# Optimization experiments

Hardware: AMD Instinct MI355X
Metric: run time of the kernel (lower is better)

## Reference

```python
import jax, jax.numpy as jnp
import numpy as np

HEADS = 12
DIM_HEAD = 64
SCALE = DIM_HEAD ** -0.5


def rotate_every_two(x):
    # (..., 2d) -> rotate pairs: (x1, x2) -> (-x2, x1)
    x = x.reshape(*x.shape[:-1], -1, 2)
    x1, x2 = x[..., 0], x[..., 1]
    return jnp.stack((-x2, x1), axis=-1).reshape(*x.shape[:-2], -1)


def apply_rotary_pos_emb(q, k, sinu_pos):
    # sinu_pos: (b, p, 2c) -> sin, cos each (b, p, c)
    b, p, two_c = sinu_pos.shape
    sp = sinu_pos.reshape(b, p, 2, two_c // 2)
    sin, cos = sp[:, :, 0, :], sp[:, :, 1, :]
    # interleave-repeat to (b, 1, p, 2c) to broadcast over heads
    sin = jnp.repeat(sin, 2, axis=-1)[:, None, :, :]
    cos = jnp.repeat(cos, 2, axis=-1)[:, None, :, :]
    rot = lambda t: t * cos + rotate_every_two(t) * sin
    return rot(q), rot(k)


def setup_inputs() -> dict:
    key = jax.random.key(0)
    ks = jax.random.split(key, 5)
    b, n, dim = 8, 1024, 768
    inner = HEADS * DIM_HEAD
    x = jax.random.normal(ks[0], (b, n, dim), dtype=jnp.float32)
    pos_emb = jax.random.normal(ks[1], (1, n, DIM_HEAD), dtype=jnp.float32)
    W_qkv = jax.random.normal(ks[2], (dim, 3 * inner), dtype=jnp.float32) * (dim ** -0.5)
    W_out = jax.random.normal(ks[3], (inner, dim), dtype=jnp.float32) * (inner ** -0.5)
    b_out = jnp.zeros((dim,), dtype=jnp.float32)
    return {"x": x, "pos_emb": pos_emb, "W_qkv": W_qkv, "W_out": W_out, "b_out": b_out}


def reference(x, pos_emb, W_qkv, W_out, b_out):
    b, n, _ = x.shape
    qkv = x @ W_qkv                                   # (b, n, 3*inner)
    q, k, v = jnp.split(qkv, 3, axis=-1)
    split_heads = lambda t: t.reshape(b, n, HEADS, DIM_HEAD).transpose(0, 2, 1, 3)
    q, k, v = split_heads(q), split_heads(k), split_heads(v)   # (b, h, n, d)
    q, k = apply_rotary_pos_emb(q, k, pos_emb)
    dots = jnp.einsum('bhid,bhjd->bhij', q, k) * SCALE
    attn = jax.nn.softmax(dots, axis=-1)
    out = jnp.einsum('bhij,bhjd->bhid', attn, v)
    out = out.transpose(0, 2, 1, 3).reshape(b, n, HEADS * DIM_HEAD)
    out = out @ W_out + b_out
    return out  # context is None -> torch code returns (out[:, :n], None); n == full length
```

## Files before the change

### kernel.cpp

```cpp
#include <hip/hip_runtime.h>
#include <hip/hip_bf16.h>

typedef __attribute__((ext_vector_type(8))) short bf16x8;
typedef __attribute__((ext_vector_type(4))) float f32x4;
typedef __attribute__((ext_vector_type(4))) unsigned short u16x4;
typedef unsigned short u16;
typedef unsigned int u32;

#define DEVINL __device__ __forceinline__

DEVINL u16 f2bf(float f) {
    union { float f; u32 u; } v; v.f = f;
    u32 r = v.u + 0x7FFFu + ((v.u >> 16) & 1u);
    return (u16)(r >> 16);
}
DEVINL float bf2f(u16 h) {
    union { u32 u; float f; } v; v.u = ((u32)h) << 16;
    return v.f;
}
DEVINL u32 cvt_pk_bf16(float lo, float hi) {
    u32 r;
    asm("v_cvt_pk_bf16_f32 %0, %1, %2" : "=v"(r) : "v"(lo), "v"(hi));
    return r;
}

#define GLOAD_LDS16(g, l) __builtin_amdgcn_global_load_lds( \
    (const __attribute__((address_space(1))) void*)(g), \
    (__attribute__((address_space(3))) void*)(l), 16, 0, 0)

#define SBAR() do { \
    __builtin_amdgcn_sched_barrier(0); \
    __builtin_amdgcn_s_barrier(); \
    __builtin_amdgcn_sched_barrier(0); } while (0)

__global__ void cvt_bf16_kernel(const float* __restrict__ in, u16* __restrict__ out, int n4) {
    int t = blockIdx.x * blockDim.x + threadIdx.x;
    if (t >= n4) return;
    const float4 v = reinterpret_cast<const float4*>(in)[t];
    u16x4 o;
    o[0] = f2bf(v.x); o[1] = f2bf(v.y); o[2] = f2bf(v.z); o[3] = f2bf(v.w);
    *reinterpret_cast<u16x4*>(out + (size_t)t * 4) = o;
}

__global__ __launch_bounds__(256) void transpose_cvt_kernel(const float* __restrict__ in,
                                                            u16* __restrict__ out,
                                                            int R, int C) {
    __shared__ float tile[32][33];
    int c0 = blockIdx.x * 32, r0 = blockIdx.y * 32;
    int tx = threadIdx.x & 31, ty = threadIdx.x >> 5;
#pragma unroll
    for (int i = 0; i < 4; ++i)
        tile[ty + i * 8][tx] = in[(size_t)(r0 + ty + i * 8) * C + c0 + tx];
    __syncthreads();
#pragma unroll
    for (int i = 0; i < 4; ++i)
        out[(size_t)(c0 + ty + i * 8) * R + r0 + tx] = f2bf(tile[tx][ty + i * 8]);
}

template<int NTN, int NFRAG, int BROWS, int K, bool BF16_OUT>
__global__ __launch_bounds__(512, 2) void gemm_bigtile_kernel(const u16* __restrict__ A,
                                                              const u16* __restrict__ Bt,
                                                              void* __restrict__ Cout,
                                                              const float* __restrict__ bias) {
    constexpr int BN = NFRAG * 32;
    constexpr int N = NTN * BN;
    constexpr int NT = K / 64;
    constexpr int APL = 256 * 64;
    constexpr int BPL = BROWS * 64;
    constexpr int BUFSZ = APL + BPL;
    constexpr int BCH = BROWS / 64;
    constexpr int TOT = 4 + BCH;
    __shared__ u16 lds[2 * BUFSZ];

    const int tid = threadIdx.x;
    const int wv = tid >> 6, lane = tid & 63;
    const int lr = lane & 15, lg = lane >> 4;
    const int wr = wv >> 1, wc = wv & 1;

    const int id = blockIdx.x;
    const int sid = (id & 7) * 32 + (id >> 3);
    const int bm = (sid / NTN) * 256;
    const int bn = (sid % NTN) * BN;

#define STAGE(nb_, kt_) do { \
    _Pragma("unroll") \
    for (int j_ = 0; j_ < 4; ++j_) { \
        const int idx_ = j_ * 512 + tid; \
        const int row_ = idx_ >> 3; \
        const int c_ = (idx_ & 7) ^ (row_ & 7); \
        GLOAD_LDS16(A + (size_t)(bm + row_) * K + (kt_) * 64 + c_ * 8, \
                    (char*)lds + ((nb_) * BUFSZ + (j_ * 512 + wv * 64) * 8) * 2); \
    } \
    _Pragma("unroll") \
    for (int j_ = 0; j_ < BCH; ++j_) { \
        const int idx_ = j_ * 512 + tid; \
        const int row_ = idx_ >> 3; \
        const int c_ = (idx_ & 7) ^ (row_ & 7); \
        GLOAD_LDS16(Bt + (size_t)(bn + row_) * K + (kt_) * 64 + c_ * 8, \
                    (char*)lds + ((nb_) * BUFSZ + APL + (j_ * 512 + wv * 64) * 8) * 2); \
    } } while (0)

#define COMPUTE(cur_) do { \
    _Pragma("unroll") \
    for (int ks_ = 0; ks_ < 2; ++ks_) { \
        bf16x8 af[4], bfr[NFRAG]; \
        _Pragma("unroll") \
        for (int mf_ = 0; mf_ < 4; ++mf_) { \
            const int row_ = wr * 64 + mf_ * 16 + lr; \
            af[mf_] = *reinterpret_cast<const bf16x8*>( \
                &lds[(cur_) * BUFSZ + row_ * 64 + (((ks_ * 4 + lg) ^ (row_ & 7)) * 8)]); \
        } \
        _Pragma("unroll") \
        for (int nf_ = 0; nf_ < NFRAG; ++nf_) { \
            const int row_ = wc * (NFRAG * 16) + nf_ * 16 + lr; \
            bfr[nf_] = *reinterpret_cast<const bf16x8*>( \
                &lds[(cur_) * BUFSZ + APL + row_ * 64 + (((ks_ * 4 + lg) ^ (row_ & 7)) * 8)]); \
        } \
        __builtin_amdgcn_s_setprio(1); \
        _Pragma("unroll") \
        for (int mf_ = 0; mf_ < 4; ++mf_) \
        _Pragma("unroll") \
        for (int nf_ = 0; nf_ < NFRAG; ++nf_) \
            acc[mf_][nf_] = __builtin_amdgcn_mfma_f32_16x16x32_bf16( \
                af[mf_], bfr[nf_], acc[mf_][nf_], 0, 0, 0); \
        __builtin_amdgcn_s_setprio(0); \
    } } while (0)

    f32x4 acc[4][NFRAG];
#pragma unroll
    for (int i = 0; i < 4; ++i)
#pragma unroll
        for (int j = 0; j < NFRAG; ++j) acc[i][j] = (f32x4){0.f, 0.f, 0.f, 0.f};

    STAGE(0, 0);
    for (int kt = 0; kt < NT - 1; ++kt) {
        const int cur = kt & 1;
        STAGE(cur ^ 1, kt + 1);
        __builtin_amdgcn_sched_barrier(0);
        if constexpr (TOT == 9) asm volatile("s_waitcnt vmcnt(9)" ::: "memory");
        else asm volatile("s_waitcnt vmcnt(6)" ::: "memory");
        SBAR();
        COMPUTE(cur);
        SBAR();
    }
    {
        const int cur = (NT - 1) & 1;
        __builtin_amdgcn_sched_barrier(0);
        asm volatile("s_waitcnt vmcnt(0)" ::: "memory");
        SBAR();
        COMPUTE(cur);
    }

#pragma unroll
    for (int mf = 0; mf < 4; ++mf)
#pragma unroll
        for (int nf = 0; nf < NFRAG; ++nf) {
            const int col = bn + wc * (NFRAG * 16) + nf * 16 + lr;
            const float bv = BF16_OUT ? 0.f : bias[col];
#pragma unroll
            for (int r = 0; r < 4; ++r) {
                const int row = bm + wr * 64 + mf * 16 + lg * 4 + r;
                if (BF16_OUT)
                    ((u16*)Cout)[(size_t)row * N + col] = f2bf(acc[mf][nf][r]);
                else
                    ((float*)Cout)[(size_t)row * N + col] = acc[mf][nf][r] + bv;
            }
        }
#undef STAGE
#undef COMPUTE
}

__global__ __launch_bounds__(256) void rot_vtrans_kernel(u16* __restrict__ qkv,
                                                         const float* __restrict__ pos,
                                                         u16* __restrict__ Vt) {
    __shared__ u16 tile[64][72];
    const int bid = blockIdx.x;
    if (bid < 6144) {
        int t = bid * 256 + threadIdx.x;
        int row = t / 192;
        int col = (t % 192) * 8;
        int n = row & 1023;
        int i0 = (col & 63) >> 1;
        const float qs = (col < 768) ? 0.18033688f : 1.0f;
        const float* pn = pos + (size_t)n * 64;
        u16* p = qkv + (size_t)row * 2304 + col;
        bf16x8 v = *reinterpret_cast<bf16x8*>(p);
        u16 o[8];
#pragma unroll
        for (int j = 0; j < 4; ++j) {
            float s = pn[i0 + j], c = pn[32 + i0 + j];
            float x0 = bf2f((u16)v[2 * j]), x1 = bf2f((u16)v[2 * j + 1]);
            o[2 * j]     = f2bf((x0 * c - x1 * s) * qs);
            o[2 * j + 1] = f2bf((x1 * c + x0 * s) * qs);
        }
        *reinterpret_cast<bf16x8*>(p) = *reinterpret_cast<bf16x8*>(o);
    } else {
        int u = bid - 6144;
        int nt = u & 15;
        int bh = u >> 4;
        int b = bh / 12, h = bh % 12;
        int tid = threadIdx.x;
        int rr = tid >> 3, cc = (tid & 7) * 8;
#pragma unroll
        for (int it = 0; it < 2; ++it) {
            int nloc = it * 32 + rr;
            const u16* src = qkv + (size_t)(b * 1024 + nt * 64 + nloc) * 2304 + 1536 + h * 64 + cc;
            bf16x8 v = *reinterpret_cast<const bf16x8*>(src);
#pragma unroll
            for (int j = 0; j < 8; ++j) tile[nloc][cc + j] = (u16)v[j];
        }
        __syncthreads();
#pragma unroll
        for (int it = 0; it < 2; ++it) {
            int d = it * 32 + rr;
            u16 o[8];
#pragma unroll
            for (int j = 0; j < 8; ++j) o[j] = tile[cc + j][d];
            *reinterpret_cast<bf16x8*>(Vt + (size_t)(bh * 64 + d) * 1024 + nt * 64 + cc) =
                *reinterpret_cast<bf16x8*>(o);
        }
    }
}

__global__ __launch_bounds__(512, 8) void attn_kernel(const u16* __restrict__ qkv,
                                                      const u16* __restrict__ Vt,
                                                      u16* __restrict__ attn_out) {
    __shared__ u16 Ks[2][64 * 64];
    __shared__ u16 Vs[2][64 * 64];
    const int d_ = blockIdx.x;
    const int bh = ((d_ >> 3) >> 3) * 8 + (d_ & 7);
    const int qt = (d_ >> 3) & 7;
    const int b = bh / 12, h = bh % 12;
    const int tid = threadIdx.x;
    const int w = tid >> 6, lr = tid & 15, lg = (tid >> 4) & 3;

    bf16x8 qf[2];
#pragma unroll
    for (int ds = 0; ds < 2; ++ds)
        qf[ds] = *reinterpret_cast<const bf16x8*>(
            &qkv[(size_t)(b * 1024 + qt * 128 + w * 16 + lr) * 2304 + h * 64 + ds * 32 + lg * 8]);

    f32x4 o[4];
#pragma unroll
    for (int i = 0; i < 4; ++i) o[i] = (f32x4){0.f, 0.f, 0.f, 0.f};
    float lsum = 0.f;

    const int srow = tid >> 3;
    const int scol = ((tid & 7) ^ (srow & 7)) * 8;
    const int srowK = (srow & 0x20) | ((srow & 0x0C) << 1) | ((srow & 0x10) >> 2) | (srow & 3);

#define STAGE_KV(nb, kt_) do { \
    GLOAD_LDS16(qkv + (size_t)(b * 1024 + (kt_) * 64 + srowK) * 2304 + 768 + h * 64 + scol, \
                (char*)Ks[nb] + tid * 16); \
    GLOAD_LDS16(Vt + (size_t)(bh * 64 + srow) * 1024 + (kt_) * 64 + scol, \
                (char*)Vs[nb] + tid * 16); \
} while (0)

    STAGE_KV(0, 0);
    __syncthreads();

    const int rsw = lr & 7;

    for (int kt = 0; kt < 16; ++kt) {
        const int cur = kt & 1;
        if (kt < 15) STAGE_KV(cur ^ 1, kt + 1);

        f32x4 s[4];
        __builtin_amdgcn_s_setprio(1);
#pragma unroll
        for (int kf = 0; kf < 4; ++kf) {
            f32x4 acc = (f32x4){0.f, 0.f, 0.f, 0.f};
#pragma unroll
            for (int ds = 0; ds < 2; ++ds) {
                bf16x8 kfr = *reinterpret_cast<const bf16x8*>(
                    &Ks[cur][(kf * 16 + lr) * 64 + (((ds * 4 + lg) ^ rsw) * 8)]);
                acc = __builtin_amdgcn_mfma_f32_16x16x32_bf16(kfr, qf[ds], acc, 0, 0, 0);
            }
            s[kf] = acc;
        }
        __builtin_amdgcn_s_setprio(0);

#pragma unroll
        for (int kf = 0; kf < 4; ++kf)
#pragma unroll
            for (int r = 0; r < 4; ++r) s[kf][r] = __builtin_amdgcn_exp2f(s[kf][r]);
        {
            float t0 = (s[0][0] + s[0][1]) + (s[0][2] + s[0][3]);
            float t1 = (s[1][0] + s[1][1]) + (s[1][2] + s[1][3]);
            float t2 = (s[2][0] + s[2][1]) + (s[2][2] + s[2][3]);
            float t3 = (s[3][0] + s[3][1]) + (s[3][2] + s[3][3]);
            lsum += (t0 + t1) + (t2 + t3);
        }

        union { u32 wd[4]; bf16x8 v; } pk[2];
#pragma unroll
        for (int ks = 0; ks < 2; ++ks) {
            pk[ks].wd[0] = cvt_pk_bf16(s[2 * ks][0], s[2 * ks][1]);
            pk[ks].wd[1] = cvt_pk_bf16(s[2 * ks][2], s[2 * ks][3]);
            pk[ks].wd[2] = cvt_pk_bf16(s[2 * ks + 1][0], s[2 * ks + 1][1]);
            pk[ks].wd[3] = cvt_pk_bf16(s[2 * ks + 1][2], s[2 * ks + 1][3]);
        }

        __builtin_amdgcn_s_setprio(1);
#pragma unroll
        for (int ks = 0; ks < 2; ++ks) {
#pragma unroll
            for (int df = 0; df < 4; ++df) {
                bf16x8 vb = *reinterpret_cast<const bf16x8*>(
                    &Vs[cur][(df * 16 + lr) * 64 + (((ks * 4 + lg) ^ rsw) * 8)]);
                o[df] = __builtin_amdgcn_mfma_f32_16x16x32_bf16(vb, pk[ks].v, o[df], 0, 0, 0);
            }
        }
        __builtin_amdgcn_s_setprio(0);
        __syncthreads();
    }
#undef STAGE_KV

    lsum += __shfl_xor(lsum, 16);
    lsum += __shfl_xor(lsum, 32);
    const float linv = 1.0f / lsum;

    u16* orow = attn_out + (size_t)(b * 1024 + qt * 128 + w * 16 + lr) * 768 + h * 64 + lg * 4;
#pragma unroll
    for (int df = 0; df < 4; ++df) {
        uint2 st;
        st.x = cvt_pk_bf16(o[df][0] * linv, o[df][1] * linv);
        st.y = cvt_pk_bf16(o[df][2] * linv, o[df][3] * linv);
        *reinterpret_cast<uint2*>(orow + df * 16) = st;
    }
}

extern "C" void kernel_launch(void* const* d_in, const int* in_sizes, int n_in,
                              void* d_out, int out_size, void* d_ws, size_t ws_size,
                              hipStream_t stream) {
    (void)in_sizes; (void)n_in; (void)out_size; (void)ws_size;
    const float* x     = (const float*)d_in[0];
    const float* pos   = (const float*)d_in[1];
    const float* W_qkv = (const float*)d_in[2];
    const float* W_out = (const float*)d_in[3];
    const float* b_out = (const float*)d_in[4];
    float* out = (float*)d_out;

    char* ws = (char*)d_ws;
    u16* xb     = (u16*)(ws);
    u16* Wqkv_t = (u16*)(ws + 12582912);
    u16* Wout_t = (u16*)(ws + 16171008);
    u16* qkv    = (u16*)(ws + 17399808);
    u16* Vt     = (u16*)(ws + 55148544);
    u16* attn_o = (u16*)(ws + 67731456);

    cvt_bf16_kernel<<<6144, 256, 0, stream>>>(x, xb, 1572864);
    transpose_cvt_kernel<<<dim3(72, 24), 256, 0, stream>>>(W_qkv, Wqkv_t, 768, 2304);
    transpose_cvt_kernel<<<dim3(24, 24), 256, 0, stream>>>(W_out, Wout_t, 768, 768);
    gemm_bigtile_kernel<8, 9, 320, 768, true><<<256, 512, 0, stream>>>(xb, Wqkv_t, qkv, nullptr);
    rot_vtrans_kernel<<<7680, 256, 0, stream>>>(qkv, pos, Vt);
    attn_kernel<<<768, 512, 0, stream>>>(qkv, Vt, attn_o);
    gemm_bigtile_kernel<8, 3, 128, 768, false><<<256, 512, 0, stream>>>(attn_o, Wout_t, out, b_out);
}
```

Baseline: 113.1 us.

## Split GEMM k-tile into half-K planes with interleaved staging and MFMA phases

Reorganizes the big-tile GEMM's LDS layout into per-32-wide-K planes, with a new swizzle suited to 32-element rows. The main loop becomes four phases: each issues part of the next tile's global-to-LDS loads, then runs a quarter of the MFMAs between barriers. The aim is to spread memory traffic across the compute and overlap loads with MFMA work more finely. In exchange there are many more barriers per k-step and more complex vmcnt accounting, which could cost as much as the overlap gains.

```diff
diff --git a/kernel.cpp b/kernel.cpp
--- a/kernel.cpp
+++ b/kernel.cpp
@@ -22,6 +22,17 @@
     u32 r;
     asm("v_cvt_pk_bf16_f32 %0, %1, %2" : "=v"(r) : "v"(lo), "v"(hi));
     return r;
+}
+
+template<int Nv> DEVINL void vmcnt_asm() {
+    if constexpr (Nv == 0) asm volatile("s_waitcnt vmcnt(0)" ::: "memory");
+    else if constexpr (Nv == 1) asm volatile("s_waitcnt vmcnt(1)" ::: "memory");
+    else if constexpr (Nv == 2) asm volatile("s_waitcnt vmcnt(2)" ::: "memory");
+    else if constexpr (Nv == 3) asm volatile("s_waitcnt vmcnt(3)" ::: "memory");
+    else if constexpr (Nv == 4) asm volatile("s_waitcnt vmcnt(4)" ::: "memory");
+    else if constexpr (Nv == 5) asm volatile("s_waitcnt vmcnt(5)" ::: "memory");
+    else if constexpr (Nv == 6) asm volatile("s_waitcnt vmcnt(6)" ::: "memory");
+    else asm volatile("s_waitcnt vmcnt(7)" ::: "memory");
 }
 
 #define GLOAD_LDS16(g, l) __builtin_amdgcn_global_load_lds( \
@@ -65,12 +76,13 @@
     constexpr int BN = NFRAG * 32;
     constexpr int N = NTN * BN;
     constexpr int NT = K / 64;
-    constexpr int APL = 256 * 64;
-    constexpr int BPL = BROWS * 64;
-    constexpr int BUFSZ = APL + BPL;
-    constexpr int BCH = BROWS / 64;
-    constexpr int TOT = 4 + BCH;
-    __shared__ u16 lds[2 * BUFSZ];
+    constexpr int PA = 256 * 32;
+    constexpr int PB = BROWS * 32;
+    constexpr int PKS = PA + PB;
+    constexpr int PBUF = 2 * PKS;
+    constexpr int BFULL = (BROWS * 4) / 512;
+    constexpr int BREM = (BROWS * 4) % 512;
+    __shared__ u16 lds[2 * PBUF];
 
     const int tid = threadIdx.x;
     const int wv = tid >> 6, lane = tid & 63;
@@ -82,73 +94,111 @@
     const int bm = (sid / NTN) * 256;
     const int bn = (sid % NTN) * BN;
 
-#define STAGE(nb_, kt_) do { \
-    _Pragma("unroll") \
-    for (int j_ = 0; j_ < 4; ++j_) { \
+#define PL(buf_, ks_, mat_) ((buf_) * PBUF + (ks_) * PKS + (mat_) * PA)
+
+#define STAGE_A(nb_, kt_, ks_) do { \
+    _Pragma("unroll") \
+    for (int j_ = 0; j_ < 2; ++j_) { \
         const int idx_ = j_ * 512 + tid; \
-        const int row_ = idx_ >> 3; \
-        const int c_ = (idx_ & 7) ^ (row_ & 7); \
-        GLOAD_LDS16(A + (size_t)(bm + row_) * K + (kt_) * 64 + c_ * 8, \
-                    (char*)lds + ((nb_) * BUFSZ + (j_ * 512 + wv * 64) * 8) * 2); \
+        const int row_ = idx_ >> 2; \
+        const int c_ = (idx_ & 3) ^ ((row_ >> 1) & 3); \
+        GLOAD_LDS16(A + (size_t)(bm + row_) * K + (kt_) * 64 + (ks_) * 32 + c_ * 8, \
+                    (char*)lds + PL((nb_), (ks_), 0) * 2 + j_ * 8192 + tid * 16); \
+    } } while (0)
+
+#define STAGE_B(nb_, kt_, ks_) do { \
+    _Pragma("unroll") \
+    for (int j_ = 0; j_ < BFULL; ++j_) { \
+        const int idx_ = j_ * 512 + tid; \
+        const int row_ = idx_ >> 2; \
+        const int c_ = (idx_ & 3) ^ ((row_ >> 1) & 3); \
+        GLOAD_LDS16(Bt + (size_t)(bn + row_) * K + (kt_) * 64 + (ks_) * 32 + c_ * 8, \
+                    (char*)lds + PL((nb_), (ks_), 1) * 2 + j_ * 8192 + tid * 16); \
     } \
-    _Pragma("unroll") \
-    for (int j_ = 0; j_ < BCH; ++j_) { \
-        const int idx_ = j_ * 512 + tid; \
-        const int row_ = idx_ >> 3; \
-        const int c_ = (idx_ & 7) ^ (row_ & 7); \
-        GLOAD_LDS16(Bt + (size_t)(bn + row_) * K + (kt_) * 64 + c_ * 8, \
-                    (char*)lds + ((nb_) * BUFSZ + APL + (j_ * 512 + wv * 64) * 8) * 2); \
+    if constexpr (BREM != 0) { \
+        if (tid < BREM) { \
+            const int idx_ = BFULL * 512 + tid; \
+            const int row_ = idx_ >> 2; \
+            const int c_ = (idx_ & 3) ^ ((row_ >> 1) & 3); \
+            GLOAD_LDS16(Bt + (size_t)(bn + row_) * K + (kt_) * 64 + (ks_) * 32 + c_ * 8, \
+                        (char*)lds + PL((nb_), (ks_), 1) * 2 + BFULL * 8192 + tid * 16); \
+        } \
     } } while (0)
 
-#define COMPUTE(cur_) do { \
-    _Pragma("unroll") \
-    for (int ks_ = 0; ks_ < 2; ++ks_) { \
-        bf16x8 af[4], bfr[NFRAG]; \
-        _Pragma("unroll") \
-        for (int mf_ = 0; mf_ < 4; ++mf_) { \
-            const int row_ = wr * 64 + mf_ * 16 + lr; \
-            af[mf_] = *reinterpret_cast<const bf16x8*>( \
-                &lds[(cur_) * BUFSZ + row_ * 64 + (((ks_ * 4 + lg) ^ (row_ & 7)) * 8)]); \
-        } \
-        _Pragma("unroll") \
-        for (int nf_ = 0; nf_ < NFRAG; ++nf_) { \
-            const int row_ = wc * (NFRAG * 16) + nf_ * 16 + lr; \
-            bfr[nf_] = *reinterpret_cast<const bf16x8*>( \
-                &lds[(cur_) * BUFSZ + APL + row_ * 64 + (((ks_ * 4 + lg) ^ (row_ & 7)) * 8)]); \
-        } \
-        __builtin_amdgcn_s_setprio(1); \
-        _Pragma("unroll") \
-        for (int mf_ = 0; mf_ < 4; ++mf_) \
-        _Pragma("unroll") \
-        for (int nf_ = 0; nf_ < NFRAG; ++nf_) \
-            acc[mf_][nf_] = __builtin_amdgcn_mfma_f32_16x16x32_bf16( \
-                af[mf_], bfr[nf_], acc[mf_][nf_], 0, 0, 0); \
-        __builtin_amdgcn_s_setprio(0); \
+#define LDA(mh_, ks_, cur_) do { \
+    _Pragma("unroll") \
+    for (int f_ = 0; f_ < 2; ++f_) { \
+        const int row_ = wr * 64 + (mh_) * 32 + f_ * 16 + lr; \
+        af[f_] = *reinterpret_cast<const bf16x8*>( \
+            &lds[PL((cur_), (ks_), 0) + row_ * 32 + ((lg ^ ((row_ >> 1) & 3)) << 3)]); \
     } } while (0)
 
+#define LDB(ks_, cur_) do { \
+    _Pragma("unroll") \
+    for (int nf_ = 0; nf_ < NFRAG; ++nf_) { \
+        const int row_ = wc * (NFRAG * 16) + nf_ * 16 + lr; \
+        bfr[nf_] = *reinterpret_cast<const bf16x8*>( \
+            &lds[PL((cur_), (ks_), 1) + row_ * 32 + ((lg ^ ((row_ >> 1) & 3)) << 3)]); \
+    } } while (0)
+
+#define MFMAQ(mh_) do { \
+    __builtin_amdgcn_s_setprio(1); \
+    _Pragma("unroll") \
+    for (int f_ = 0; f_ < 2; ++f_) \
+    _Pragma("unroll") \
+    for (int nf_ = 0; nf_ < NFRAG; ++nf_) \
+        acc[(mh_) * 2 + f_][nf_] = __builtin_amdgcn_mfma_f32_16x16x32_bf16( \
+            af[f_], bfr[nf_], acc[(mh_) * 2 + f_][nf_], 0, 0, 0); \
+    __builtin_amdgcn_s_setprio(0); } while (0)
+
+#define WAITHALF() do { \
+    __builtin_amdgcn_sched_barrier(0); \
+    if constexpr (BREM != 0) { \
+        if (wv < BREM / 64) vmcnt_asm<2 + BFULL + 1>(); \
+        else vmcnt_asm<2 + BFULL>(); \
+    } else { \
+        vmcnt_asm<2 + BFULL>(); \
+    } } while (0)
+
     f32x4 acc[4][NFRAG];
 #pragma unroll
     for (int i = 0; i < 4; ++i)
 #pragma unroll
         for (int j = 0; j < NFRAG; ++j) acc[i][j] = (f32x4){0.f, 0.f, 0.f, 0.f};
 
-    STAGE(0, 0);
+    bf16x8 af[2], bfr[NFRAG];
+
+    STAGE_A(0, 0, 0); STAGE_B(0, 0, 0); STAGE_A(0, 0, 1); STAGE_B(0, 0, 1);
+    __builtin_amdgcn_sched_barrier(0);
+    vmcnt_asm<0>();
+    SBAR();
+
     for (int kt = 0; kt < NT - 1; ++kt) {
-        const int cur = kt & 1;
-        STAGE(cur ^ 1, kt + 1);
-        __builtin_amdgcn_sched_barrier(0);
-        if constexpr (TOT == 9) asm volatile("s_waitcnt vmcnt(9)" ::: "memory");
-        else asm volatile("s_waitcnt vmcnt(6)" ::: "memory");
-        SBAR();
-        COMPUTE(cur);
-        SBAR();
+        const int cur = kt & 1, nxt = cur ^ 1;
+        LDB(0, cur); LDA(0, 0, cur);
+        STAGE_A(nxt, kt + 1, 0);
+        SBAR(); MFMAQ(0); SBAR();
+        LDA(1, 0, cur);
+        STAGE_B(nxt, kt + 1, 0);
+        WAITHALF();
+        SBAR(); MFMAQ(1); SBAR();
+        LDB(1, cur); LDA(0, 1, cur);
+        STAGE_A(nxt, kt + 1, 1);
+        SBAR(); MFMAQ(0); SBAR();
+        LDA(1, 1, cur);
+        STAGE_B(nxt, kt + 1, 1);
+        WAITHALF();
+        SBAR(); MFMAQ(1); SBAR();
     }
     {
         const int cur = (NT - 1) & 1;
+        LDB(0, cur); LDA(0, 0, cur); SBAR(); MFMAQ(0); SBAR();
+        LDA(1, 0, cur);
         __builtin_amdgcn_sched_barrier(0);
-        asm volatile("s_waitcnt vmcnt(0)" ::: "memory");
-        SBAR();
-        COMPUTE(cur);
+        vmcnt_asm<0>();
+        SBAR(); MFMAQ(1); SBAR();
+        LDB(1, cur); LDA(0, 1, cur); SBAR(); MFMAQ(0); SBAR();
+        LDA(1, 1, cur); SBAR(); MFMAQ(1);
     }
 
 #pragma unroll
@@ -166,8 +216,13 @@
                     ((float*)Cout)[(size_t)row * N + col] = acc[mf][nf][r] + bv;
             }
         }
-#undef STAGE
-#undef COMPUTE
+#undef PL
+#undef STAGE_A
+#undef STAGE_B
+#undef LDA
+#undef LDB
+#undef MFMAQ
+#undef WAITHALF
 }
 
 __global__ __launch_bounds__(256) void rot_vtrans_kernel(u16* __restrict__ qkv,
```

Result: no change. 115.3 us (+2.0%).
